# Kernel optimization log

Measured on AMD Instinct MI355X. Metric: run time of the kernel, lower is better.

The kernel has to match this reference:

```python
import jax, jax.numpy as jnp
import numpy as np

D = 1024      # EMBEDDING_DIM
H = 16        # ATTENTION_HEADS
HD = 64       # HEAD_DIM
B, S = 4, 2048
EPS = 1e-5


def setup_inputs() -> dict:
    key = jax.random.key(0)
    ks = jax.random.split(key, 16)
    std = 0.02
    inp = {
        "x": jax.random.normal(ks[0], (B, S, D), dtype=jnp.float32),
        # per-head Q/K/V weights stacked: [H, D, HD]
        "Wq": jax.random.normal(ks[1], (H, D, HD), dtype=jnp.float32) * std,
        "Wk": jax.random.normal(ks[2], (H, D, HD), dtype=jnp.float32) * std,
        "Wv": jax.random.normal(ks[3], (H, D, HD), dtype=jnp.float32) * std,
        "bq": jnp.zeros((H, HD), dtype=jnp.float32),
        "bk": jnp.zeros((H, HD), dtype=jnp.float32),
        "bv": jnp.zeros((H, HD), dtype=jnp.float32),
        "Wo": jax.random.normal(ks[4], (D, D), dtype=jnp.float32) * std,
        "bo": jnp.zeros((D,), dtype=jnp.float32),
        "W1": jax.random.normal(ks[5], (D, 4 * D), dtype=jnp.float32) * std,
        "b1": jnp.zeros((4 * D,), dtype=jnp.float32),
        "W2": jax.random.normal(ks[6], (4 * D, D), dtype=jnp.float32) * std,
        "b2": jnp.zeros((D,), dtype=jnp.float32),
        # single shared LayerNorm (same module used for both pre-norms)
        "gamma": jnp.ones((D,), dtype=jnp.float32),
        "beta": jnp.zeros((D,), dtype=jnp.float32),
    }
    return inp


def _layer_norm(x, gamma, beta):
    mu = jnp.mean(x, axis=-1, keepdims=True)
    var = jnp.mean(jnp.square(x - mu), axis=-1, keepdims=True)
    return (x - mu) * jax.lax.rsqrt(var + EPS) * gamma + beta


def _block(x, Wq, Wk, Wv, bq, bk, bv, Wo, bo, W1, b1, W2, b2, gamma, beta):
    # pre-norm attention
    h = _layer_norm(x, gamma, beta)                     # [B,S,D]
    Q = jnp.einsum('bsd,hdk->bhsk', h, Wq) + bq[None, :, None, :]
    K = jnp.einsum('bsd,hdk->bhsk', h, Wk) + bk[None, :, None, :]
    V = jnp.einsum('bsd,hdk->bhsk', h, Wv) + bv[None, :, None, :]
    scores = jnp.einsum('bhsk,bhtk->bhst', Q, K) / jnp.sqrt(jnp.float32(HD))
    causal = jnp.tril(jnp.ones((S, S), dtype=bool))     # True = keep
    scores = jnp.where(causal[None, None], scores, -jnp.inf)
    attn = jax.nn.softmax(scores, axis=-1)              # [B,H,S,S]
    out = jnp.einsum('bhst,bhtk->bhsk', attn, V)        # [B,H,S,HD]
    out = out.transpose(0, 2, 1, 3).reshape(x.shape[0], x.shape[1], D)
    x = x + out @ Wo + bo
    # pre-norm MLP (shared layer norm params)
    h2 = _layer_norm(x, gamma, beta)
    mlp = jax.nn.gelu(h2 @ W1 + b1, approximate=False) @ W2 + b2
    return x + mlp


def reference(x, Wq, Wk, Wv, bq, bk, bv, Wo, bo, W1, b1, W2, b2, gamma, beta):
    return _block(x, Wq, Wk, Wv, bq, bk, bv, Wo, bo, W1, b1, W2, b2, gamma, beta)
```

## Files before the change

### kernel.cpp

```cpp
#include <hip/hip_runtime.h>
#include <hip/hip_bf16.h>

typedef __bf16  bf16x8 __attribute__((ext_vector_type(8)));
typedef float   f32x4  __attribute__((ext_vector_type(4)));
typedef short   s16x8  __attribute__((ext_vector_type(8)));

typedef const __attribute__((address_space(1))) void g_void;
typedef __attribute__((address_space(3))) void l_void;

__device__ __forceinline__ short f2b(float x) {
    __hip_bfloat16 h = __float2bfloat16(x);
    return __builtin_bit_cast(short, h);
}

__device__ __forceinline__ int pk2(float lo, float hi) {
    return (int)(unsigned short)f2b(lo) | ((int)f2b(hi) << 16);
}

__device__ __forceinline__ float fast_gelu(float v) {
    const float a = fminf(2.3022082f * (v + 0.044715f * v * v * v), 126.0f);
    const float t = exp2f(a);
    return v * t / (t + 1.0f);
}

__device__ __forceinline__ f32x4 mfma16(s16x8 a, s16x8 b, f32x4 c) {
    return __builtin_amdgcn_mfma_f32_16x16x32_bf16(
        __builtin_bit_cast(bf16x8, a), __builtin_bit_cast(bf16x8, b), c, 0, 0, 0);
}

__global__ __launch_bounds__(256) void transpose_bf16(
    const float* __restrict__ src, short* __restrict__ dst, int R, int C) {
    __shared__ float tile[32][33];
    src += (size_t)blockIdx.z * R * C;
    dst += (size_t)blockIdx.z * R * C;
    const int c0 = blockIdx.x * 32, r0 = blockIdx.y * 32;
    const int tx = threadIdx.x & 31, ty = threadIdx.x >> 5;
#pragma unroll
    for (int i = 0; i < 32; i += 8)
        tile[ty + i][tx] = src[(size_t)(r0 + ty + i) * C + c0 + tx];
    __syncthreads();
#pragma unroll
    for (int i = 0; i < 32; i += 8)
        dst[(size_t)(c0 + ty + i) * R + r0 + tx] = f2b(tile[tx][ty + i]);
}

__global__ __launch_bounds__(256) void concat_bias(
    const float* __restrict__ bq, const float* __restrict__ bk,
    const float* __restrict__ bv, float* __restrict__ o) {
    int i = blockIdx.x * 256 + threadIdx.x;
    if (i < 1024)      o[i] = bq[i];
    else if (i < 2048) o[i] = bk[i - 1024];
    else if (i < 3072) o[i] = bv[i - 2048];
}

__global__ __launch_bounds__(256) void ln_bf16(
    const float* __restrict__ x, const float* __restrict__ gamma,
    const float* __restrict__ beta, short* __restrict__ out) {
    __shared__ float red[8];
    const int row = blockIdx.x, tid = threadIdx.x;
    const float4 v = *(const float4*)(x + (size_t)row * 1024 + tid * 4);
    float s = v.x + v.y + v.z + v.w;
    float q = v.x * v.x + v.y * v.y + v.z * v.z + v.w * v.w;
#pragma unroll
    for (int off = 32; off > 0; off >>= 1) {
        s += __shfl_xor(s, off);
        q += __shfl_xor(q, off);
    }
    if ((tid & 63) == 0) { red[(tid >> 6) * 2] = s; red[(tid >> 6) * 2 + 1] = q; }
    __syncthreads();
    s = red[0] + red[2] + red[4] + red[6];
    q = red[1] + red[3] + red[5] + red[7];
    const float mu = s * (1.0f / 1024.0f);
    const float var = q * (1.0f / 1024.0f) - mu * mu;
    const float rs = rsqrtf(var + 1e-5f);
    const float4 g  = *(const float4*)(gamma + tid * 4);
    const float4 bt = *(const float4*)(beta + tid * 4);
    short4 o;
    o.x = f2b((v.x - mu) * rs * g.x + bt.x);
    o.y = f2b((v.y - mu) * rs * g.y + bt.y);
    o.z = f2b((v.z - mu) * rs * g.z + bt.z);
    o.w = f2b((v.w - mu) * rs * g.w + bt.w);
    *(short4*)(out + (size_t)row * 1024 + tid * 4) = o;
}

template <int MODE>
__global__ __launch_bounds__(512) void gemm_bf16(
    const short* __restrict__ A, const short* __restrict__ Bt,
    const float* __restrict__ bias, const float* __restrict__ resid,
    float* __restrict__ outf, short* __restrict__ outb, short* __restrict__ vt,
    int M, int N, int K) {
    __shared__ __align__(16) short As[2 * 128 * 32];
    __shared__ __align__(16) short Bs[2 * 128 * 32];

    const int tid = threadIdx.x;
    const int wave = tid >> 6, lane = tid & 63;
    const int l16 = lane & 15, quad = lane >> 4;
    const int wm = wave & 3, wn = wave >> 2;
    const int gx = gridDim.x;
    const int g = blockIdx.y * gx + blockIdx.x;
    const int xcd = g & 7, s = g >> 3;
    const int mband = gridDim.y >> 3;
    const int sm = s / gx;
    const int m0 = (xcd * mband + sm) * 128;
    const int n0 = (s - sm * gx) * 128;
    const int lrow = lane >> 2;
    const int lcol = (lane & 3) * 8;

    f32x4 acc[2][4] = {};

    for (int kk = 0; kk < K; kk += 64) {
#pragma unroll
        for (int p = 0; p < 2; ++p) {
            const int r = wave * 16 + lrow;
            const short* ga = A + (size_t)(m0 + r) * K + kk + p * 32 + lcol;
            short* la = &As[p * 4096 + wave * 512];
            __builtin_amdgcn_global_load_lds((g_void*)ga, (l_void*)la, 16, 0, 0);
            const short* gb = Bt + (size_t)(n0 + r) * K + kk + p * 32 + lcol;
            short* lb = &Bs[p * 4096 + wave * 512];
            __builtin_amdgcn_global_load_lds((g_void*)gb, (l_void*)lb, 16, 0, 0);
        }
        __syncthreads();
#pragma unroll
        for (int p = 0; p < 2; ++p) {
            s16x8 a[2], b[4];
#pragma unroll
            for (int t = 0; t < 2; ++t)
                a[t] = *(const s16x8*)&As[p * 4096 + (wm * 32 + t * 16 + l16) * 32 + quad * 8];
#pragma unroll
            for (int t = 0; t < 4; ++t)
                b[t] = *(const s16x8*)&Bs[p * 4096 + (wn * 64 + t * 16 + l16) * 32 + quad * 8];
#pragma unroll
            for (int mt = 0; mt < 2; ++mt)
#pragma unroll
                for (int nt = 0; nt < 4; ++nt)
                    acc[mt][nt] = mfma16(a[mt], b[nt], acc[mt][nt]);
        }
        __syncthreads();
    }

#pragma unroll
    for (int mt = 0; mt < 2; ++mt) {
#pragma unroll
        for (int nt = 0; nt < 4; ++nt) {
            const int row = m0 + wm * 32 + mt * 16 + quad * 4;
            const int col = n0 + wn * 64 + nt * 16 + l16;
            const float bc = bias[col];
            float v[4];
#pragma unroll
            for (int r = 0; r < 4; ++r) v[r] = acc[mt][nt][r] + bc;

            if (MODE == 0) {
                const int sel = col >> 10, within = col & 1023;
                const int h = within >> 6, hd = within & 63;
                const size_t bidx = (size_t)row >> 11, sp = row & 2047;
                if (sel == 0) {
#pragma unroll
                    for (int r = 0; r < 4; ++r) v[r] *= 0.18033688011112042f;
                }
                if (sel < 2) {
#pragma unroll
                    for (int r = 0; r < 4; ++r)
                        outb[(size_t)sel * (8192ull * 1024) +
                             ((bidx * 16 + h) * 2048 + sp + r) * 64 + hd] = f2b(v[r]);
                } else {
                    short4 o4;
                    o4.x = f2b(v[0]); o4.y = f2b(v[1]);
                    o4.z = f2b(v[2]); o4.w = f2b(v[3]);
                    *(short4*)&vt[((bidx * 16 + h) * 64 + hd) * 2048 + sp] = o4;
                }
            } else if (MODE == 1) {
#pragma unroll
                for (int r = 0; r < 4; ++r) {
                    const size_t rr = (size_t)(row + r);
                    outf[rr * N + col] = v[r] + resid[rr * N + col];
                }
            } else {
#pragma unroll
                for (int r = 0; r < 4; ++r)
                    outb[(size_t)(row + r) * N + col] = f2b(fast_gelu(v[r]));
            }
        }
    }
}

__global__ __launch_bounds__(256) void attn_kernel(
    const short* __restrict__ Q, const short* __restrict__ K,
    const short* __restrict__ Vt, short* __restrict__ O) {
    const int bid = blockIdx.x;
    const int p = bid & 15;
    const int h = (bid >> 4) & 15;
    const int b = bid >> 8;
    const int tid = threadIdx.x, wave = tid >> 6, lane = tid & 63;
    const int l16 = lane & 15, quad = lane >> 4;

    __shared__ __align__(16) short Ks[64 * 72];
    __shared__ __align__(16) short Vts[64 * 72];
    __shared__ __align__(16) short Ps[4][16 * 72];

    const size_t bh = ((size_t)b * 16 + h) * (2048ull * 64);
    const int srow = tid >> 2;
    const int sseg = (tid & 3) * 16;

    for (int pass = 0; pass < 2; ++pass) {
        const int qt = pass ? (31 - p) : p;
        const int q0 = qt * 64;
        const int q_lane = q0 + wave * 16 + l16;

        const short* qrow = Q + bh + (size_t)q_lane * 64;
        s16x8 bq0 = *(const s16x8*)(qrow + quad * 8);
        s16x8 bq1 = *(const s16x8*)(qrow + 32 + quad * 8);

        f32x4 oacc[4] = {};
        float lsum = 0.0f;

        s16x8 k0, k1, v0, v1;
        {
            const short* kg = K + bh + (size_t)srow * 64 + sseg;
            k0 = *(const s16x8*)kg;
            k1 = *(const s16x8*)(kg + 8);
            const short* vg = Vt + bh + (size_t)srow * 2048 + sseg;
            v0 = *(const s16x8*)vg;
            v1 = *(const s16x8*)(vg + 8);
        }

        for (int j = 0; j <= qt; ++j) {
            __syncthreads();
            *(s16x8*)&Ks[srow * 72 + sseg]      = k0;
            *(s16x8*)&Ks[srow * 72 + sseg + 8]  = k1;
            *(s16x8*)&Vts[srow * 72 + sseg]     = v0;
            *(s16x8*)&Vts[srow * 72 + sseg + 8] = v1;
            __syncthreads();

            if (j < qt) {
                const short* kg = K + bh + (size_t)((j + 1) * 64 + srow) * 64 + sseg;
                k0 = *(const s16x8*)kg;
                k1 = *(const s16x8*)(kg + 8);
                const short* vg = Vt + bh + (size_t)srow * 2048 + (j + 1) * 64 + sseg;
                v0 = *(const s16x8*)vg;
                v1 = *(const s16x8*)(vg + 8);
            }

            f32x4 st[4];
#pragma unroll
            for (int s = 0; s < 4; ++s) {
                s16x8 ak0 = *(const s16x8*)&Ks[(s * 16 + l16) * 72 + quad * 8];
                s16x8 ak1 = *(const s16x8*)&Ks[(s * 16 + l16) * 72 + 32 + quad * 8];
                f32x4 c = {};
                c = mfma16(ak0, bq0, c);
                c = mfma16(ak1, bq1, c);
                st[s] = c;
            }
            if (j == qt) {
#pragma unroll
                for (int s = 0; s < 4; ++s)
#pragma unroll
                    for (int r = 0; r < 4; ++r) {
                        const int t = j * 64 + s * 16 + quad * 4 + r;
                        if (t > q_lane) st[s][r] = -3000.0f;
                    }
            }
            float rs = 0.0f;
#pragma unroll
            for (int s = 0; s < 4; ++s) {
#pragma unroll
                for (int r = 0; r < 4; ++r) {
                    st[s][r] = exp2f(st[s][r]);
                    rs += st[s][r];
                }
                int2 pw;
                pw.x = pk2(st[s][0], st[s][1]);
                pw.y = pk2(st[s][2], st[s][3]);
                *(int2*)&Ps[wave][l16 * 72 + s * 16 + quad * 4] = pw;
            }
            rs += __shfl_xor(rs, 16);
            rs += __shfl_xor(rs, 32);
            lsum += rs;

            asm volatile("s_waitcnt lgkmcnt(0)" ::: "memory");
            s16x8 ap0 = *(const s16x8*)&Ps[wave][l16 * 72 + quad * 8];
            s16x8 ap1 = *(const s16x8*)&Ps[wave][l16 * 72 + 32 + quad * 8];

#pragma unroll
            for (int nt = 0; nt < 4; ++nt) {
                s16x8 bv0 = *(const s16x8*)&Vts[(nt * 16 + l16) * 72 + quad * 8];
                s16x8 bv1 = *(const s16x8*)&Vts[(nt * 16 + l16) * 72 + 32 + quad * 8];
                oacc[nt] = mfma16(ap0, bv0, oacc[nt]);
                oacc[nt] = mfma16(ap1, bv1, oacc[nt]);
            }
        }
        __syncthreads();

        float inv[4];
#pragma unroll
        for (int r = 0; r < 4; ++r)
            inv[r] = 1.0f / __shfl(lsum, quad * 4 + r, 64);
#pragma unroll
        for (int nt = 0; nt < 4; ++nt)
#pragma unroll
            for (int r = 0; r < 4; ++r) {
                const int row = q0 + wave * 16 + quad * 4 + r;
                O[((size_t)b * 2048 + row) * 1024 + h * 64 + nt * 16 + l16] =
                    f2b(oacc[nt][r] * inv[r]);
            }
    }
}

extern "C" void kernel_launch(void* const* d_in, const int* in_sizes, int n_in,
                              void* d_out, int out_size, void* d_ws, size_t ws_size,
                              hipStream_t stream) {
    const float* x     = (const float*)d_in[0];
    const float* Wq    = (const float*)d_in[1];
    const float* Wk    = (const float*)d_in[2];
    const float* Wv    = (const float*)d_in[3];
    const float* bq    = (const float*)d_in[4];
    const float* bk    = (const float*)d_in[5];
    const float* bv    = (const float*)d_in[6];
    const float* Wo    = (const float*)d_in[7];
    const float* bo    = (const float*)d_in[8];
    const float* W1    = (const float*)d_in[9];
    const float* b1    = (const float*)d_in[10];
    const float* W2    = (const float*)d_in[11];
    const float* b2    = (const float*)d_in[12];
    const float* gamma = (const float*)d_in[13];
    const float* beta  = (const float*)d_in[14];
    float* out = (float*)d_out;

    char* ws = (char*)d_ws;
    size_t off = 0;
    auto alloc = [&](size_t bytes) -> char* {
        char* p = ws + off;
        off += (bytes + 255) & ~(size_t)255;
        return p;
    };
    short* h1    = (short*)alloc(8192ull * 1024 * 2);
    short* btqkv = (short*)alloc(3072ull * 1024 * 2);
    short* btwo  = (short*)alloc(1024ull * 1024 * 2);
    short* btw1  = (short*)alloc(4096ull * 1024 * 2);
    short* btw2  = (short*)alloc(1024ull * 4096 * 2);
    float* bqkv  = (float*)alloc(3072ull * 4);
    short* qkv   = (short*)alloc(2ull * 8192 * 1024 * 2);
    short* vt    = (short*)alloc(8192ull * 1024 * 2);
    short* aout  = (short*)alloc(8192ull * 1024 * 2);
    float* x2    = (float*)alloc(8192ull * 1024 * 4);
    short* h2    = (short*)alloc(8192ull * 1024 * 2);
    short* m1    = (short*)alloc(8192ull * 4096 * 2);

    transpose_bf16<<<dim3(2, 32, 16), 256, 0, stream>>>(Wq, btqkv, 1024, 64);
    transpose_bf16<<<dim3(2, 32, 16), 256, 0, stream>>>(Wk, btqkv + 1024ull * 1024, 1024, 64);
    transpose_bf16<<<dim3(2, 32, 16), 256, 0, stream>>>(Wv, btqkv + 2ull * 1024 * 1024, 1024, 64);
    transpose_bf16<<<dim3(32, 32, 1), 256, 0, stream>>>(Wo, btwo, 1024, 1024);
    transpose_bf16<<<dim3(128, 32, 1), 256, 0, stream>>>(W1, btw1, 1024, 4096);
    transpose_bf16<<<dim3(32, 128, 1), 256, 0, stream>>>(W2, btw2, 4096, 1024);
    concat_bias<<<12, 256, 0, stream>>>(bq, bk, bv, bqkv);

    ln_bf16<<<8192, 256, 0, stream>>>(x, gamma, beta, h1);
    gemm_bf16<0><<<dim3(24, 64), 512, 0, stream>>>(
        h1, btqkv, bqkv, nullptr, nullptr, qkv, vt, 8192, 3072, 1024);
    attn_kernel<<<1024, 256, 0, stream>>>(
        qkv, qkv + 8192ull * 1024, vt, aout);
    gemm_bf16<1><<<dim3(8, 64), 512, 0, stream>>>(
        aout, btwo, bo, x, x2, nullptr, nullptr, 8192, 1024, 1024);
    ln_bf16<<<8192, 256, 0, stream>>>(x2, gamma, beta, h2);
    gemm_bf16<2><<<dim3(32, 64), 512, 0, stream>>>(
        h2, btw1, b1, nullptr, nullptr, m1, nullptr, 8192, 4096, 1024);
    gemm_bf16<1><<<dim3(8, 64), 512, 0, stream>>>(
        m1, btw2, b2, x2, out, nullptr, nullptr, 8192, 1024, 4096);
}
```

Measured before the change: 517.7 us.

## Swizzle GEMM tiles by N band and give attention blocks four balanced query tiles

```diff
diff --git a/kernel.cpp b/kernel.cpp
--- a/kernel.cpp
+++ b/kernel.cpp
@@ -99,10 +99,11 @@
     const int gx = gridDim.x;
     const int g = blockIdx.y * gx + blockIdx.x;
     const int xcd = g & 7, s = g >> 3;
-    const int mband = gridDim.y >> 3;
-    const int sm = s / gx;
-    const int m0 = (xcd * mband + sm) * 128;
-    const int n0 = (s - sm * gx) * 128;
+    const int nband = gx >> 3;
+    const int sm = s / nband;
+    const int sn = s - sm * nband;
+    const int m0 = sm * 128;
+    const int n0 = (xcd * nband + sn) * 128;
     const int lrow = lane >> 2;
     const int lcol = (lane & 3) * 8;
 
@@ -187,22 +188,24 @@
     const short* __restrict__ Q, const short* __restrict__ K,
     const short* __restrict__ Vt, short* __restrict__ O) {
     const int bid = blockIdx.x;
-    const int p = bid & 15;
-    const int h = (bid >> 4) & 15;
-    const int b = bid >> 8;
+    const int gq = bid & 7;
+    const int h  = (bid >> 3) & 15;
+    const int b  = bid >> 7;
     const int tid = threadIdx.x, wave = tid >> 6, lane = tid & 63;
     const int l16 = lane & 15, quad = lane >> 4;
 
-    __shared__ __align__(16) short Ks[64 * 72];
-    __shared__ __align__(16) short Vts[64 * 72];
+    __shared__ __align__(16) short Ks[2][64 * 72];
+    __shared__ __align__(16) short Vts[2][64 * 72];
     __shared__ __align__(16) short Ps[4][16 * 72];
 
     const size_t bh = ((size_t)b * 16 + h) * (2048ull * 64);
     const int srow = tid >> 2;
     const int sseg = (tid & 3) * 16;
 
-    for (int pass = 0; pass < 2; ++pass) {
-        const int qt = pass ? (31 - p) : p;
+    const int qts[4] = {gq, 15 - gq, 16 + gq, 31 - gq};
+
+    for (int pass = 0; pass < 4; ++pass) {
+        const int qt = qts[pass];
         const int q0 = qt * 64;
         const int q_lane = q0 + wave * 16 + l16;
 
@@ -224,11 +227,11 @@
         }
 
         for (int j = 0; j <= qt; ++j) {
-            __syncthreads();
-            *(s16x8*)&Ks[srow * 72 + sseg]      = k0;
-            *(s16x8*)&Ks[srow * 72 + sseg + 8]  = k1;
-            *(s16x8*)&Vts[srow * 72 + sseg]     = v0;
-            *(s16x8*)&Vts[srow * 72 + sseg + 8] = v1;
+            const int buf = j & 1;
+            *(s16x8*)&Ks[buf][srow * 72 + sseg]      = k0;
+            *(s16x8*)&Ks[buf][srow * 72 + sseg + 8]  = k1;
+            *(s16x8*)&Vts[buf][srow * 72 + sseg]     = v0;
+            *(s16x8*)&Vts[buf][srow * 72 + sseg + 8] = v1;
             __syncthreads();
 
             if (j < qt) {
@@ -243,8 +246,8 @@
             f32x4 st[4];
 #pragma unroll
             for (int s = 0; s < 4; ++s) {
-                s16x8 ak0 = *(const s16x8*)&Ks[(s * 16 + l16) * 72 + quad * 8];
-                s16x8 ak1 = *(const s16x8*)&Ks[(s * 16 + l16) * 72 + 32 + quad * 8];
+                s16x8 ak0 = *(const s16x8*)&Ks[buf][(s * 16 + l16) * 72 + quad * 8];
+                s16x8 ak1 = *(const s16x8*)&Ks[buf][(s * 16 + l16) * 72 + 32 + quad * 8];
                 f32x4 c = {};
                 c = mfma16(ak0, bq0, c);
                 c = mfma16(ak1, bq1, c);
@@ -282,8 +285,8 @@
 
 #pragma unroll
             for (int nt = 0; nt < 4; ++nt) {
-                s16x8 bv0 = *(const s16x8*)&Vts[(nt * 16 + l16) * 72 + quad * 8];
-                s16x8 bv1 = *(const s16x8*)&Vts[(nt * 16 + l16) * 72 + 32 + quad * 8];
+                s16x8 bv0 = *(const s16x8*)&Vts[buf][(nt * 16 + l16) * 72 + quad * 8];
+                s16x8 bv1 = *(const s16x8*)&Vts[buf][(nt * 16 + l16) * 72 + 32 + quad * 8];
                 oacc[nt] = mfma16(ap0, bv0, oacc[nt]);
                 oacc[nt] = mfma16(ap1, bv1, oacc[nt]);
             }
@@ -356,7 +359,7 @@
     ln_bf16<<<8192, 256, 0, stream>>>(x, gamma, beta, h1);
     gemm_bf16<0><<<dim3(24, 64), 512, 0, stream>>>(
         h1, btqkv, bqkv, nullptr, nullptr, qkv, vt, 8192, 3072, 1024);
-    attn_kernel<<<1024, 256, 0, stream>>>(
+    attn_kernel<<<512, 256, 0, stream>>>(
         qkv, qkv + 8192ull * 1024, vt, aout);
     gemm_bf16<1><<<dim3(8, 64), 512, 0, stream>>>(
         aout, btwo, bo, x, x2, nullptr, nullptr, 8192, 1024, 1024);
```

Result: no change. 519.9 us (+0.4%).
